# Kernel tuning notes

Hardware: AMD Instinct MI355X
Metric: run time of the kernel (lower is better)

Reference implementation:

```python
import jax, jax.numpy as jnp
import numpy as np

B, C_IN, C_OUT, N = 8, 256, 128, 4096
BN_EPS = 1e-5


def _conv1x1(w, b, t):
    # w: [out, in], t: [B, in, N] -> [B, out, N]
    return jnp.einsum('oc,bcn->bon', w, t) + b[None, :, None]


def setup_inputs() -> dict:
    key = jax.random.key(0)
    ks = jax.random.split(key, 11)
    s_in = 1.0 / np.sqrt(C_IN)
    s_out = 1.0 / np.sqrt(C_OUT)
    return {
        'x': jax.random.normal(ks[0], (B, C_IN, N), dtype=jnp.float32),
        'g_w': jax.random.normal(ks[1], (C_OUT, C_IN), dtype=jnp.float32) * s_in,
        'g_b': jax.random.normal(ks[2], (C_OUT,), dtype=jnp.float32) * s_in,
        'theta_w': jax.random.normal(ks[3], (C_OUT, C_IN), dtype=jnp.float32) * s_in,
        'theta_b': jax.random.normal(ks[4], (C_OUT,), dtype=jnp.float32) * s_in,
        'phi_w': jax.random.normal(ks[5], (C_OUT, C_IN), dtype=jnp.float32) * s_in,
        'phi_b': jax.random.normal(ks[6], (C_OUT,), dtype=jnp.float32) * s_in,
        'W_w': jax.random.normal(ks[7], (C_IN, C_OUT), dtype=jnp.float32) * s_out,
        'W_b': jax.random.normal(ks[8], (C_IN,), dtype=jnp.float32) * s_out,
        'bn_gamma': jax.random.uniform(ks[9], (C_IN,), dtype=jnp.float32),
        'bn_beta': jax.random.normal(ks[10], (C_IN,), dtype=jnp.float32) * 0.1,
    }


def reference(x, g_w, g_b, theta_w, theta_b, phi_w, phi_b, W_w, W_b, bn_gamma, bn_beta):
    n = x.shape[-1]
    g_x = _conv1x1(g_w, g_b, x)          # [B, Co, N]
    theta_x = _conv1x1(theta_w, theta_b, x)  # [B, Co, N]
    phi_x = _conv1x1(phi_w, phi_b, x)        # [B, Co, N]
    # f = theta_x^T @ phi_x, divided by N (no softmax) -> [B, N, N]
    f_div_c = jnp.einsum('bcn,bcm->bnm', theta_x, phi_x) / n
    # y[b,c,n] = sum_m f[b,n,m] * g_x[b,c,m]  -> already permuted to [B, Co, N]
    y = jnp.einsum('bnm,bcm->bcn', f_div_c, g_x)
    w_y = jnp.einsum('oc,bcn->bon', W_w, y) + W_b[None, :, None]  # [B, C_in, N]
    # BatchNorm1d, training mode: stats over (batch, spatial), biased variance
    mean = w_y.mean(axis=(0, 2), keepdims=True)
    var = w_y.var(axis=(0, 2), keepdims=True)
    w_y = (w_y - mean) * jax.lax.rsqrt(var + BN_EPS)
    w_y = w_y * bn_gamma[None, :, None] + bn_beta[None, :, None]
    return w_y + x  # generate=True residual
```

## Files before the change

kernel.cpp:

```cpp
#include <hip/hip_runtime.h>
#include <hip/hip_bf16.h>
#include <stdint.h>

#define BB   8
#define CIN  256
#define COUT 128
#define NN   4096

using f32x4  = __attribute__((ext_vector_type(4))) float;
using bf16x8 = __attribute__((ext_vector_type(8))) __bf16;
using u16x8  = __attribute__((ext_vector_type(8))) unsigned short;

static __device__ __forceinline__ unsigned short f2bf(float f) {
    unsigned int u = __builtin_bit_cast(unsigned int, f);
    u += 0x7FFFu + ((u >> 16) & 1u);
    return (unsigned short)(u >> 16);
}
static __device__ __forceinline__ float bf2f(unsigned short u) {
    return __builtin_bit_cast(float, (unsigned int)u << 16);
}
static __device__ __forceinline__ ushort4 pack4(float a, float b, float c, float d) {
    ushort4 r; r.x=f2bf(a); r.y=f2bf(b); r.z=f2bf(c); r.w=f2bf(d); return r;
}
static __device__ __forceinline__ bf16x8 pack8(float4 a, float4 b) {
    u16x8 r;
    r[0]=f2bf(a.x); r[1]=f2bf(a.y); r[2]=f2bf(a.z); r[3]=f2bf(a.w);
    r[4]=f2bf(b.x); r[5]=f2bf(b.y); r[6]=f2bf(b.z); r[7]=f2bf(b.w);
    return __builtin_bit_cast(bf16x8, r);
}
#define MFMA(a,b,c) __builtin_amdgcn_mfma_f32_16x16x32_bf16((a),(b),(c),0,0,0)

static __device__ __forceinline__ int sw64(int r, int c)  { return (r*64  + c) ^ ((r&7)<<3); }

typedef __attribute__((address_space(3))) unsigned int lds_uint;
typedef __attribute__((address_space(1))) const unsigned int glob_uint;
static __device__ __forceinline__ void glds16(const void* g, void* l) {
    __builtin_amdgcn_global_load_lds((glob_uint*)g, (lds_uint*)l, 16, 0, 0);
}

__global__ __launch_bounds__(256) void z0_prep(
    const float* __restrict__ gw, const float* __restrict__ pw, const float* __restrict__ tw,
    const float* __restrict__ gb, const float* __restrict__ pb, const float* __restrict__ tb,
    float* __restrict__ M1, float* __restrict__ stats,
    unsigned short* __restrict__ Wcat, float* __restrict__ biascat)
{
    int t = blockIdx.x * 256 + threadIdx.x;
    int gs = gridDim.x * 256;
    float4 z = {0.f,0.f,0.f,0.f};
    for (int i = t; i < 32768 + 128; i += gs) {
        if (i < 32768) ((float4*)M1)[i] = z;
        else ((float4*)stats)[i - 32768] = z;
    }
    for (int i = t; i < 24576; i += gs) {
        int flat = i * 4;
        int o = flat >> 8, c = flat & 255;
        const float* src = (o < 128) ? (gw + o*256) : (o < 256) ? (pw + (o-128)*256) : (tw + (o-256)*256);
        float4 f = *(const float4*)(src + c);
        ushort4 u; u.x=f2bf(f.x); u.y=f2bf(f.y); u.z=f2bf(f.z); u.w=f2bf(f.w);
        *(ushort4*)(Wcat + flat) = u;
    }
    if (t < 384)
        biascat[t] = (t < 128) ? gb[t] : (t < 256) ? pb[t-128] : tb[t-256];
}

__global__ __launch_bounds__(512) void k1_conv3(
    const float* __restrict__ x, const unsigned short* __restrict__ Wcat,
    const float* __restrict__ biascat,
    unsigned short* __restrict__ G, unsigned short* __restrict__ P,
    unsigned short* __restrict__ TT)
{
    __shared__ __align__(16) unsigned short Xs[128*256];
    int b  = blockIdx.x >> 5;
    int n0 = (blockIdx.x & 31) * 128;
    int t  = threadIdx.x;

    {
        int c  = t & 255;
        int nq = (t >> 8) * 64;
        const float* xp = x + ((size_t)b*CIN + c)*NN + n0 + nq;
        #pragma unroll
        for (int r = 0; r < 16; ++r) {
            float4 f = *(const float4*)(xp + r*4);
            int n = nq + r*4;
            Xs[(n+0)*256 + (c ^ (((n+0)&7)<<3))] = f2bf(f.x);
            Xs[(n+1)*256 + (c ^ (((n+1)&7)<<3))] = f2bf(f.y);
            Xs[(n+2)*256 + (c ^ (((n+2)&7)<<3))] = f2bf(f.z);
            Xs[(n+3)*256 + (c ^ (((n+3)&7)<<3))] = f2bf(f.w);
        }
    }
    __syncthreads();

    int lane = t & 63, wv = t >> 6;
    int wr = wv >> 2, wc = wv & 3;
    int lr = lane & 15, lg = lane >> 4;
    int nb = wr*64, ob = wc*96;

    f32x4 acc[4][6];
    #pragma unroll
    for (int i=0;i<4;i++)
        #pragma unroll
        for (int j=0;j<6;j++) acc[i][j] = (f32x4){0.f,0.f,0.f,0.f};

    #pragma unroll
    for (int ks = 0; ks < 8; ++ks) {
        bf16x8 xf[4], wf[6];
        #pragma unroll
        for (int ni = 0; ni < 4; ++ni) {
            int n = nb + ni*16 + lr;
            int cq = (ks*4 + lg) ^ (n & 7);
            xf[ni] = __builtin_bit_cast(bf16x8, *(const u16x8*)&Xs[n*256 + cq*8]);
        }
        #pragma unroll
        for (int os = 0; os < 6; ++os) {
            int o = ob + os*16 + lr;
            wf[os] = __builtin_bit_cast(bf16x8, *(const u16x8*)(Wcat + (size_t)o*256 + ks*32 + lg*8));
        }
        #pragma unroll
        for (int os = 0; os < 6; ++os) {
            bool th = (ob + os*16) >= 256;
            #pragma unroll
            for (int ni = 0; ni < 4; ++ni)
                acc[ni][os] = th ? MFMA(wf[os], xf[ni], acc[ni][os])
                                 : MFMA(xf[ni], wf[os], acc[ni][os]);
        }
    }

    unsigned short* Gb  = G  + (size_t)b*COUT*NN;
    unsigned short* Pb  = P  + (size_t)b*COUT*NN;
    unsigned short* TTb = TT + (size_t)b*NN*COUT;
    #pragma unroll
    for (int os = 0; os < 6; ++os) {
        int o = ob + os*16;
        if (o < 256) {
            float bv = biascat[o + lr];
            unsigned short* dst = ((o < 128) ? (Gb + (size_t)(o + lr)*NN)
                                             : (Pb + (size_t)(o - 128 + lr)*NN)) + n0 + nb;
            #pragma unroll
            for (int ni = 0; ni < 4; ++ni) {
                f32x4 v = acc[ni][os];
                *(ushort4*)(dst + ni*16 + lg*4) = pack4(v[0]+bv, v[1]+bv, v[2]+bv, v[3]+bv);
            }
        } else {
            int c0 = o - 256 + lg*4;
            float b0 = biascat[o + lg*4 + 0];
            float b1 = biascat[o + lg*4 + 1];
            float b2 = biascat[o + lg*4 + 2];
            float b3 = biascat[o + lg*4 + 3];
            #pragma unroll
            for (int ni = 0; ni < 4; ++ni) {
                int n = n0 + nb + ni*16 + lr;
                f32x4 v = acc[ni][os];
                *(ushort4*)(TTb + (size_t)n*COUT + c0) = pack4(v[0]+b0, v[1]+b1, v[2]+b2, v[3]+b3);
            }
        }
    }
}

__global__ __launch_bounds__(256) void k2_m1(
    const unsigned short* __restrict__ P, const unsigned short* __restrict__ G,
    float* __restrict__ M1)
{
    __shared__ __align__(16) unsigned short Ps[128*64];
    __shared__ __align__(16) unsigned short Gs[128*64];
    int b  = blockIdx.x >> 4;
    int ks = blockIdx.x & 15;
    int t = threadIdx.x;
    int lane = t & 63, wv = t >> 6;
    int wr = wv >> 1, wc = wv & 1;
    int lr = lane & 15, lg = lane >> 4;

    f32x4 acc[4][4];
    #pragma unroll
    for (int i=0;i<4;i++)
        #pragma unroll
        for (int j=0;j<4;j++) acc[i][j] = (f32x4){0.f,0.f,0.f,0.f};

    const unsigned short* Pb = P + (size_t)b*COUT*NN;
    const unsigned short* Gb = G + (size_t)b*COUT*NN;

    for (int it = 0; it < 4; ++it) {
        int n0 = ks*256 + it*64;
        #pragma unroll
        for (int ss = 0; ss < 4; ++ss) {
            int idx = ss*256 + t;
            int row = idx >> 3;
            int c8  = (idx & 7) * 8;
            u16x8 v = *(const u16x8*)(Pb + (size_t)row*NN + n0 + c8);
            *(u16x8*)&Ps[sw64(row, c8)] = v;
            u16x8 g = *(const u16x8*)(Gb + (size_t)row*NN + n0 + c8);
            *(u16x8*)&Gs[sw64(row, c8)] = g;
        }
        __syncthreads();
        #pragma unroll
        for (int kk = 0; kk < 2; ++kk) {
            bf16x8 af[4], bfr[4];
            #pragma unroll
            for (int mi=0; mi<4; ++mi) {
                int row = wr*64 + mi*16 + lr;
                af[mi] = __builtin_bit_cast(bf16x8, *(const u16x8*)&Ps[sw64(row, kk*32 + lg*8)]);
            }
            #pragma unroll
            for (int ni=0; ni<4; ++ni) {
                int row = wc*64 + ni*16 + lr;
                bfr[ni] = __builtin_bit_cast(bf16x8, *(const u16x8*)&Gs[sw64(row, kk*32 + lg*8)]);
            }
            #pragma unroll
            for (int mi=0; mi<4; ++mi)
                #pragma unroll
                for (int ni=0; ni<4; ++ni)
                    acc[mi][ni] = MFMA(af[mi], bfr[ni], acc[mi][ni]);
        }
        __syncthreads();
    }
    float* m1b = M1 + (size_t)b*16384;
    #pragma unroll
    for (int mi=0; mi<4; ++mi)
        #pragma unroll
        for (int j=0; j<4; ++j) {
            int kch = wr*64 + mi*16 + lg*4 + j;
            #pragma unroll
            for (int ni=0; ni<4; ++ni) {
                int cch = wc*64 + ni*16 + lr;
                atomicAdd(&m1b[kch*128 + cch], acc[mi][ni][j]);
            }
        }
}

__global__ __launch_bounds__(256) void k3_w2(
    const float* __restrict__ Ww, const float* __restrict__ M1,
    unsigned short* __restrict__ W2)
{
    int b = blockIdx.x >> 2, q = blockIdx.x & 3;
    int wv = threadIdx.x >> 6, lane = threadIdx.x & 63;
    int lr = lane & 15, lg = lane >> 4;
    int o16 = q*64 + wv*16;

    bf16x8 a[4];
    const float* wrow = Ww + (size_t)(o16 + lr)*128;
    #pragma unroll
    for (int ksx=0; ksx<4; ++ksx) {
        float4 f0 = *(const float4*)(wrow + ksx*32 + lg*8);
        float4 f1 = *(const float4*)(wrow + ksx*32 + lg*8 + 4);
        a[ksx] = pack8(f0, f1);
    }
    const float* m1b = M1 + (size_t)b*16384;
    for (int kt = 0; kt < 8; ++kt) {
        f32x4 acc = (f32x4){0.f,0.f,0.f,0.f};
        const float* mrow = m1b + (size_t)(kt*16 + lr)*128;
        #pragma unroll
        for (int ksx=0; ksx<4; ++ksx) {
            float4 f0 = *(const float4*)(mrow + ksx*32 + lg*8);
            float4 f1 = *(const float4*)(mrow + ksx*32 + lg*8 + 4);
            bf16x8 bb = pack8(f0, f1);
            acc = MFMA(a[ksx], bb, acc);
        }
        #pragma unroll
        for (int j=0;j<4;++j) {
            int o = o16 + lg*4 + j;
            int k = kt*16 + lr;
            W2[(size_t)b*32768 + (size_t)o*128 + k] = f2bf(acc[j] * (1.0f/4096.0f));
        }
    }
}

__global__ __launch_bounds__(512) void k4_wy(
    const unsigned short* __restrict__ W2, const unsigned short* __restrict__ TT,
    const float* __restrict__ Wb, unsigned short* __restrict__ WY,
    float* __restrict__ stats)
{
    __shared__ __align__(16) unsigned short Ts[128*128];
    __shared__ float sb[512];
    int b  = blockIdx.x >> 5;
    int n0 = (blockIdx.x & 31) * 128;
    int t  = threadIdx.x;
    int lane = t & 63, wv = t >> 6;
    sb[t] = 0.f;

    const unsigned short* TTb = TT + ((size_t)b*NN + n0)*COUT;
    #pragma unroll
    for (int g = 0; g < 4; ++g) {
        int nl = wv*16 + g*4 + (lane >> 4);
        int kq = lane & 15;
        const unsigned short* src = TTb + (size_t)nl*128 + ((kq ^ (nl & 7)) * 8);
        glds16(src, &Ts[(wv*16 + g*4) * 128]);
    }
    asm volatile("s_waitcnt vmcnt(0)");
    __syncthreads();

    int wr = wv >> 2, wo = wv & 3;
    int lr = lane & 15, lg = lane >> 4;
    int nb = wr*64, ob = wo*64;
    const unsigned short* W2b = W2 + (size_t)b*32768;

    f32x4 acc[4][4];
    #pragma unroll
    for (int i=0;i<4;i++)
        #pragma unroll
        for (int j=0;j<4;j++) acc[i][j] = (f32x4){0.f,0.f,0.f,0.f};

    #pragma unroll
    for (int ks = 0; ks < 4; ++ks) {
        bf16x8 tf[4], wf[4];
        #pragma unroll
        for (int ni = 0; ni < 4; ++ni) {
            int n = nb + ni*16 + lr;
            int kq = (ks*4 + lg) ^ (n & 7);
            tf[ni] = __builtin_bit_cast(bf16x8, *(const u16x8*)&Ts[n*128 + kq*8]);
        }
        #pragma unroll
        for (int oi = 0; oi < 4; ++oi) {
            int o = ob + oi*16 + lr;
            wf[oi] = __builtin_bit_cast(bf16x8, *(const u16x8*)(W2b + (size_t)o*128 + ks*32 + lg*8));
        }
        #pragma unroll
        for (int ni = 0; ni < 4; ++ni)
            #pragma unroll
            for (int oi = 0; oi < 4; ++oi)
                acc[ni][oi] = MFMA(tf[ni], wf[oi], acc[ni][oi]);
    }

    unsigned short* wyb = WY + (size_t)b*CIN*NN;
    #pragma unroll
    for (int oi = 0; oi < 4; ++oi) {
        int o = ob + oi*16 + lr;
        float bv = Wb[o];
        float s1 = 0.f, s2 = 0.f;
        #pragma unroll
        for (int ni = 0; ni < 4; ++ni) {
            f32x4 v = acc[ni][oi];
            float v0 = v[0]+bv, v1 = v[1]+bv, v2 = v[2]+bv, v3 = v[3]+bv;
            s1 += v0+v1+v2+v3;
            s2 += v0*v0+v1*v1+v2*v2+v3*v3;
            *(ushort4*)(wyb + (size_t)o*NN + n0 + nb + ni*16 + lg*4) = pack4(v0,v1,v2,v3);
        }
        s1 += __shfl_xor(s1, 16); s1 += __shfl_xor(s1, 32);
        s2 += __shfl_xor(s2, 16); s2 += __shfl_xor(s2, 32);
        if (lg == 0) {
            atomicAdd(&sb[o], s1);
            atomicAdd(&sb[256 + o], s2);
        }
    }
    __syncthreads();
    atomicAdd(&stats[t], sb[t]);
}

__global__ __launch_bounds__(256) void k6_final(
    const unsigned short* __restrict__ WY, const float* __restrict__ x,
    const float* __restrict__ stats, const float* __restrict__ gamma,
    const float* __restrict__ beta, float* __restrict__ out)
{
    const float inv = 1.0f / (float)(BB * NN);
    int stride = gridDim.x * blockDim.x;
    for (int i = blockIdx.x * blockDim.x + threadIdx.x; i < (BB*CIN*NN)/8; i += stride) {
        int c = (i >> 9) & 255;
        float mean = stats[c] * inv;
        float var  = stats[256 + c] * inv - mean*mean;
        float sc   = gamma[c] * rsqrtf(var + 1e-5f);
        float bb   = beta[c];
        u16x8 w = ((const u16x8*)WY)[i];
        float4 x0 = ((const float4*)x)[i*2];
        float4 x1 = ((const float4*)x)[i*2+1];
        float4 r0, r1;
        r0.x = (bf2f(w[0]) - mean)*sc + bb + x0.x;
        r0.y = (bf2f(w[1]) - mean)*sc + bb + x0.y;
        r0.z = (bf2f(w[2]) - mean)*sc + bb + x0.z;
        r0.w = (bf2f(w[3]) - mean)*sc + bb + x0.w;
        r1.x = (bf2f(w[4]) - mean)*sc + bb + x1.x;
        r1.y = (bf2f(w[5]) - mean)*sc + bb + x1.y;
        r1.z = (bf2f(w[6]) - mean)*sc + bb + x1.z;
        r1.w = (bf2f(w[7]) - mean)*sc + bb + x1.w;
        ((float4*)out)[i*2]   = r0;
        ((float4*)out)[i*2+1] = r1;
    }
}

extern "C" void kernel_launch(void* const* d_in, const int* in_sizes, int n_in,
                              void* d_out, int out_size, void* d_ws, size_t ws_size,
                              hipStream_t stream)
{
    (void)in_sizes; (void)n_in; (void)out_size; (void)ws_size;
    const float* x     = (const float*)d_in[0];
    const float* gw    = (const float*)d_in[1];
    const float* gb    = (const float*)d_in[2];
    const float* tw    = (const float*)d_in[3];
    const float* tb    = (const float*)d_in[4];
    const float* pw    = (const float*)d_in[5];
    const float* pb    = (const float*)d_in[6];
    const float* Ww    = (const float*)d_in[7];
    const float* Wb    = (const float*)d_in[8];
    const float* gamma = (const float*)d_in[9];
    const float* beta  = (const float*)d_in[10];
    float* out = (float*)d_out;

    char* ws = (char*)d_ws;
    unsigned short* G    = (unsigned short*)(ws + 0);
    unsigned short* P    = (unsigned short*)(ws + (8u<<20));
    unsigned short* WY   = (unsigned short*)(ws + 0);
    unsigned short* TT   = (unsigned short*)(ws + (16u<<20));
    float* M1            = (float*)(ws + (24u<<20));
    unsigned short* W2   = (unsigned short*)(ws + (24u<<20) + 524288);
    unsigned short* Wcat = (unsigned short*)(ws + (25u<<20));
    float* biascat       = (float*)(ws + (25u<<20) + 196608);
    float* stats         = (float*)(ws + (25u<<20) + 198656);

    z0_prep <<<128,  256, 0, stream>>>(gw, pw, tw, gb, pb, tb, M1, stats, Wcat, biascat);
    k1_conv3<<<256,  512, 0, stream>>>(x, Wcat, biascat, G, P, TT);
    k2_m1   <<<128,  256, 0, stream>>>(P, G, M1);
    k3_w2   <<<32,   256, 0, stream>>>(Ww, M1, W2);
    k4_wy   <<<256,  512, 0, stream>>>(W2, TT, Wb, WY, stats);
    k6_final<<<2048, 256, 0, stream>>>(WY, x, stats, gamma, beta, out);
}
```

Baseline: 98.90 us.

## Replace M1 atomics with partial buffers, vectorize x transpose, use direct-to-LDS loads

k2_m1 now writes each block's partial M1 to its own slice instead of issuing float atomicAdds, and k3_w2 sums the 16 partials per batch into LDS before the MFMA step. This also removes the M1 zeroing from z0_prep. k1_conv3 loads four channels at a time so it can write packed ushort4 to LDS instead of scalar stores. k2_m1 stages tiles with global_load_lds. The cost is more workspace, a k3 launch of only 8 blocks that must read 8 MB of partials, and less parallelism in k3.

```diff
diff --git a/kernel.cpp b/kernel.cpp
--- a/kernel.cpp
+++ b/kernel.cpp
@@ -41,16 +41,11 @@
 __global__ __launch_bounds__(256) void z0_prep(
     const float* __restrict__ gw, const float* __restrict__ pw, const float* __restrict__ tw,
     const float* __restrict__ gb, const float* __restrict__ pb, const float* __restrict__ tb,
-    float* __restrict__ M1, float* __restrict__ stats,
+    float* __restrict__ stats,
     unsigned short* __restrict__ Wcat, float* __restrict__ biascat)
 {
     int t = blockIdx.x * 256 + threadIdx.x;
     int gs = gridDim.x * 256;
-    float4 z = {0.f,0.f,0.f,0.f};
-    for (int i = t; i < 32768 + 128; i += gs) {
-        if (i < 32768) ((float4*)M1)[i] = z;
-        else ((float4*)stats)[i - 32768] = z;
-    }
     for (int i = t; i < 24576; i += gs) {
         int flat = i * 4;
         int o = flat >> 8, c = flat & 255;
@@ -59,6 +54,7 @@
         ushort4 u; u.x=f2bf(f.x); u.y=f2bf(f.y); u.z=f2bf(f.z); u.w=f2bf(f.w);
         *(ushort4*)(Wcat + flat) = u;
     }
+    if (t < 512) stats[t] = 0.f;
     if (t < 384)
         biascat[t] = (t < 128) ? gb[t] : (t < 256) ? pb[t-128] : tb[t-256];
 }
@@ -75,17 +71,21 @@
     int t  = threadIdx.x;
 
     {
-        int c  = t & 255;
-        int nq = (t >> 8) * 64;
-        const float* xp = x + ((size_t)b*CIN + c)*NN + n0 + nq;
-        #pragma unroll
-        for (int r = 0; r < 16; ++r) {
-            float4 f = *(const float4*)(xp + r*4);
-            int n = nq + r*4;
-            Xs[(n+0)*256 + (c ^ (((n+0)&7)<<3))] = f2bf(f.x);
-            Xs[(n+1)*256 + (c ^ (((n+1)&7)<<3))] = f2bf(f.y);
-            Xs[(n+2)*256 + (c ^ (((n+2)&7)<<3))] = f2bf(f.z);
-            Xs[(n+3)*256 + (c ^ (((n+3)&7)<<3))] = f2bf(f.w);
+        int nq = (t & 31) * 4;
+        int c0 = (t >> 5) * 4;
+        const float* xb = x + (size_t)b*CIN*NN + n0 + nq;
+        #pragma unroll
+        for (int p = 0; p < 4; ++p) {
+            int c = p*64 + c0;
+            const float* xp = xb + (size_t)c*NN;
+            float4 f0 = *(const float4*)(xp);
+            float4 f1 = *(const float4*)(xp + NN);
+            float4 f2 = *(const float4*)(xp + 2*NN);
+            float4 f3 = *(const float4*)(xp + 3*NN);
+            *(ushort4*)&Xs[(nq+0)*256 + (c ^ (((nq+0)&7)<<3))] = pack4(f0.x,f1.x,f2.x,f3.x);
+            *(ushort4*)&Xs[(nq+1)*256 + (c ^ (((nq+1)&7)<<3))] = pack4(f0.y,f1.y,f2.y,f3.y);
+            *(ushort4*)&Xs[(nq+2)*256 + (c ^ (((nq+2)&7)<<3))] = pack4(f0.z,f1.z,f2.z,f3.z);
+            *(ushort4*)&Xs[(nq+3)*256 + (c ^ (((nq+3)&7)<<3))] = pack4(f0.w,f1.w,f2.w,f3.w);
         }
     }
     __syncthreads();
@@ -158,12 +158,13 @@
 
 __global__ __launch_bounds__(256) void k2_m1(
     const unsigned short* __restrict__ P, const unsigned short* __restrict__ G,
-    float* __restrict__ M1)
+    float* __restrict__ M1p)
 {
     __shared__ __align__(16) unsigned short Ps[128*64];
     __shared__ __align__(16) unsigned short Gs[128*64];
-    int b  = blockIdx.x >> 4;
-    int ks = blockIdx.x & 15;
+    int bid = blockIdx.x;
+    int b  = bid >> 4;
+    int ks = bid & 15;
     int t = threadIdx.x;
     int lane = t & 63, wv = t >> 6;
     int wr = wv >> 1, wc = wv & 1;
@@ -181,15 +182,14 @@
     for (int it = 0; it < 4; ++it) {
         int n0 = ks*256 + it*64;
         #pragma unroll
-        for (int ss = 0; ss < 4; ++ss) {
-            int idx = ss*256 + t;
-            int row = idx >> 3;
-            int c8  = (idx & 7) * 8;
-            u16x8 v = *(const u16x8*)(Pb + (size_t)row*NN + n0 + c8);
-            *(u16x8*)&Ps[sw64(row, c8)] = v;
-            u16x8 g = *(const u16x8*)(Gb + (size_t)row*NN + n0 + c8);
-            *(u16x8*)&Gs[sw64(row, c8)] = g;
-        }
+        for (int g4 = 0; g4 < 4; ++g4) {
+            int row0 = wv*32 + g4*8;
+            int row  = row0 + (lane >> 3);
+            int gg   = (lane & 7) ^ (row & 7);
+            glds16(Pb + (size_t)row*NN + n0 + gg*8, &Ps[row0*64]);
+            glds16(Gb + (size_t)row*NN + n0 + gg*8, &Gs[row0*64]);
+        }
+        asm volatile("s_waitcnt vmcnt(0)");
         __syncthreads();
         #pragma unroll
         for (int kk = 0; kk < 2; ++kk) {
@@ -212,7 +212,7 @@
         }
         __syncthreads();
     }
-    float* m1b = M1 + (size_t)b*16384;
+    float* dst = M1p + (size_t)bid*16384;
     #pragma unroll
     for (int mi=0; mi<4; ++mi)
         #pragma unroll
@@ -221,44 +221,59 @@
             #pragma unroll
             for (int ni=0; ni<4; ++ni) {
                 int cch = wc*64 + ni*16 + lr;
-                atomicAdd(&m1b[kch*128 + cch], acc[mi][ni][j]);
-            }
-        }
-}
-
-__global__ __launch_bounds__(256) void k3_w2(
-    const float* __restrict__ Ww, const float* __restrict__ M1,
+                dst[kch*128 + cch] = acc[mi][ni][j];
+            }
+        }
+}
+
+__global__ __launch_bounds__(512) void k3_w2(
+    const float* __restrict__ Ww, const float* __restrict__ M1p,
     unsigned short* __restrict__ W2)
 {
-    int b = blockIdx.x >> 2, q = blockIdx.x & 3;
-    int wv = threadIdx.x >> 6, lane = threadIdx.x & 63;
+    __shared__ float Ms[16384];
+    int b = blockIdx.x;
+    int t = threadIdx.x;
+
+    for (int i4 = t; i4 < 4096; i4 += 512) {
+        float4 s = {0.f,0.f,0.f,0.f};
+        #pragma unroll
+        for (int p = 0; p < 16; ++p) {
+            float4 v = ((const float4*)(M1p + (size_t)(b*16 + p)*16384))[i4];
+            s.x += v.x; s.y += v.y; s.z += v.z; s.w += v.w;
+        }
+        int k = i4 >> 5, q = i4 & 31;
+        *(float4*)&Ms[k*128 + ((q ^ (k&7)) * 4)] = s;
+    }
+    __syncthreads();
+
+    int lane = t & 63, wv = t >> 6;
     int lr = lane & 15, lg = lane >> 4;
-    int o16 = q*64 + wv*16;
-
-    bf16x8 a[4];
-    const float* wrow = Ww + (size_t)(o16 + lr)*128;
-    #pragma unroll
-    for (int ksx=0; ksx<4; ++ksx) {
-        float4 f0 = *(const float4*)(wrow + ksx*32 + lg*8);
-        float4 f1 = *(const float4*)(wrow + ksx*32 + lg*8 + 4);
-        a[ksx] = pack8(f0, f1);
-    }
-    const float* m1b = M1 + (size_t)b*16384;
-    for (int kt = 0; kt < 8; ++kt) {
-        f32x4 acc = (f32x4){0.f,0.f,0.f,0.f};
-        const float* mrow = m1b + (size_t)(kt*16 + lr)*128;
+    #pragma unroll
+    for (int oo = 0; oo < 2; ++oo) {
+        int o16 = oo*128 + wv*16;
+        bf16x8 a[4];
+        const float* wrow = Ww + (size_t)(o16 + lr)*128;
         #pragma unroll
         for (int ksx=0; ksx<4; ++ksx) {
-            float4 f0 = *(const float4*)(mrow + ksx*32 + lg*8);
-            float4 f1 = *(const float4*)(mrow + ksx*32 + lg*8 + 4);
-            bf16x8 bb = pack8(f0, f1);
-            acc = MFMA(a[ksx], bb, acc);
-        }
-        #pragma unroll
-        for (int j=0;j<4;++j) {
-            int o = o16 + lg*4 + j;
+            float4 f0 = *(const float4*)(wrow + ksx*32 + lg*8);
+            float4 f1 = *(const float4*)(wrow + ksx*32 + lg*8 + 4);
+            a[ksx] = pack8(f0, f1);
+        }
+        for (int kt = 0; kt < 8; ++kt) {
+            f32x4 acc = (f32x4){0.f,0.f,0.f,0.f};
             int k = kt*16 + lr;
-            W2[(size_t)b*32768 + (size_t)o*128 + k] = f2bf(acc[j] * (1.0f/4096.0f));
+            #pragma unroll
+            for (int ksx=0; ksx<4; ++ksx) {
+                int q0 = ksx*8 + lg*2;
+                float4 f0 = *(const float4*)&Ms[k*128 + ((q0     ^ (k&7)) * 4)];
+                float4 f1 = *(const float4*)&Ms[k*128 + (((q0+1) ^ (k&7)) * 4)];
+                acc = MFMA(a[ksx], pack8(f0, f1), acc);
+            }
+            #pragma unroll
+            for (int j=0;j<4;++j) {
+                int o = o16 + lg*4 + j;
+                W2[(size_t)b*32768 + (size_t)o*128 + (kt*16 + lr)] = f2bf(acc[j] * (1.0f/4096.0f));
+            }
         }
     }
 }
@@ -397,16 +412,16 @@
     unsigned short* P    = (unsigned short*)(ws + (8u<<20));
     unsigned short* WY   = (unsigned short*)(ws + 0);
     unsigned short* TT   = (unsigned short*)(ws + (16u<<20));
-    float* M1            = (float*)(ws + (24u<<20));
-    unsigned short* W2   = (unsigned short*)(ws + (24u<<20) + 524288);
-    unsigned short* Wcat = (unsigned short*)(ws + (25u<<20));
-    float* biascat       = (float*)(ws + (25u<<20) + 196608);
-    float* stats         = (float*)(ws + (25u<<20) + 198656);
-
-    z0_prep <<<128,  256, 0, stream>>>(gw, pw, tw, gb, pb, tb, M1, stats, Wcat, biascat);
+    float* M1p           = (float*)(ws + (24u<<20));
+    unsigned short* W2   = (unsigned short*)(ws + (32u<<20));
+    unsigned short* Wcat = (unsigned short*)(ws + (33u<<20));
+    float* biascat       = (float*)(ws + (33u<<20) + 196608);
+    float* stats         = (float*)(ws + (33u<<20) + 198656);
+
+    z0_prep <<<96,   256, 0, stream>>>(gw, pw, tw, gb, pb, tb, stats, Wcat, biascat);
     k1_conv3<<<256,  512, 0, stream>>>(x, Wcat, biascat, G, P, TT);
-    k2_m1   <<<128,  256, 0, stream>>>(P, G, M1);
-    k3_w2   <<<32,   256, 0, stream>>>(Ww, M1, W2);
+    k2_m1   <<<128,  256, 0, stream>>>(P, G, M1p);
+    k3_w2   <<<8,    512, 0, stream>>>(Ww, M1p, W2);
     k4_wy   <<<256,  512, 0, stream>>>(W2, TT, Wb, WY, stats);
     k6_final<<<2048, 256, 0, stream>>>(WY, x, stats, gamma, beta, out);
 }
```

Result: faster. 96.35 us (-2.6%).
